# Performance work log

Measured on AMD Instinct MI355X. Metric: run time of the kernel, lower is better.

Reference implementation:

```python
import jax, jax.numpy as jnp
import numpy as np

N_NODES = 150000   # node_num
N_CENTROIDS = 256  # in_feats (must equal out_feats per source view())
EMBED = 256        # out_feats
EPS = 1e-7


def setup_inputs() -> dict:
    key = jax.random.key(0)
    k1, k2, k3 = jax.random.split(key, 3)
    x = jax.random.normal(k1, (N_NODES, EMBED), dtype=jnp.float32)
    # project node representations strictly inside the unit Poincare ball
    x = x / (1.0 + jnp.linalg.norm(x, axis=-1, keepdims=True)) * 0.9
    mask = (jax.random.uniform(k2, (N_NODES, 1)) < 0.9).astype(jnp.float32)
    # centroid_embedding init: uniform(-0.01, 0.01), already well inside the ball
    w = jax.random.uniform(k3, (N_CENTROIDS, EMBED), minval=-0.01, maxval=0.01,
                           dtype=jnp.float32)
    return {"node_repr": x, "mask": mask, "centroid_weight": w}


def _poincare_pairwise(x, c):
    # x: [N, D] inside unit ball, c: [C, D] inside unit ball -> [N, C]
    sx = jnp.sum(x * x, axis=-1)              # [N]
    sc = jnp.sum(c * c, axis=-1)              # [C]
    xc = x @ c.T                               # [N, C] (the only GEMM)
    sq = jnp.maximum(sx[:, None] + sc[None, :] - 2.0 * xc, 0.0)  # ||x-y||^2
    denom = jnp.maximum((1.0 - sx)[:, None] * (1.0 - sc)[None, :], 1e-12)
    arg = 1.0 + 2.0 * sq / denom
    return jnp.arccosh(jnp.maximum(arg, 1.0 + EPS))


def reference(node_repr, mask, centroid_weight):
    # node_repr: [N, D], mask: [N, 1], centroid_weight: [C, D]
    d = _poincare_pairwise(node_repr, centroid_weight)     # [N, C]
    node_centroid_dist = d[None, :, :] * mask              # [1, N, C] (mask broadcasts)
    graph_centroid_dist = jnp.sum(node_centroid_dist, axis=1) / jnp.sum(mask)  # [1, C]
    return graph_centroid_dist, node_centroid_dist
```

## Files before the change

kernel.cpp:

```cpp
#include <hip/hip_runtime.h>
#include <hip/hip_bf16.h>

#define N_NODES 150000
#define CDIM 256
#define DIM 256

typedef float f32x4 __attribute__((ext_vector_type(4)));
typedef short bf16x8 __attribute__((ext_vector_type(8)));

#define WS_CB 0
#define WS_SC 131072
#define WS_GACC 132096
#define WS_MSUM 133120

__device__ __forceinline__ unsigned short f2bf(float f) {
  unsigned u = __float_as_uint(f);
  u += 0x7FFFu + ((u >> 16) & 1u);
  return (unsigned short)(u >> 16);
}

__global__ void cd_prep(const float* __restrict__ cw, const float* __restrict__ mask,
                        unsigned short* __restrict__ cb, float* __restrict__ sc,
                        float* __restrict__ msum) {
  int b = blockIdx.x;
  int t = threadIdx.x;
  int wave = t >> 6, lane = t & 63;
  __shared__ float red[4];
  if (b < CDIM) {
    float v = cw[b * DIM + t];
    cb[(size_t)(t >> 3) * (CDIM * 8) + b * 8 + (t & 7)] = f2bf(v);
    float ss = v * v;
    #pragma unroll
    for (int off = 32; off >= 1; off >>= 1) ss += __shfl_xor(ss, off);
    if (lane == 0) red[wave] = ss;
    __syncthreads();
    if (t == 0) sc[b] = red[0] + red[1] + red[2] + red[3];
  } else {
    int idx = (b - CDIM) * 256 + t;
    const int stride = 64 * 256;
    float s = 0.f;
    for (int i = idx; i < N_NODES; i += stride) s += mask[i];
    #pragma unroll
    for (int off = 32; off >= 1; off >>= 1) s += __shfl_xor(s, off);
    if (lane == 0) red[wave] = s;
    __syncthreads();
    if (t == 0) atomicAdd(msum, red[0] + red[1] + red[2] + red[3]);
  }
}

__global__ __launch_bounds__(256, 2)
void cd_main(const float* __restrict__ x, const float* __restrict__ mask,
             const unsigned short* __restrict__ cb, const float* __restrict__ sc,
             float* __restrict__ gacc, float* __restrict__ out1) {
  const int lane = threadIdx.x & 63;
  const int w = threadIdx.x >> 6;
  const int q = lane >> 4;
  const int ln = lane & 15;
  const long m0 = (long)blockIdx.x * 64;
  const int c0 = w * 64;

  f32x4 acc[4][4] = {};
  float spart[4] = {0.f, 0.f, 0.f, 0.f};

  for (int kt = 0; kt < 8; ++kt) {
    bf16x8 bf[4];
    #pragma unroll
    for (int nt = 0; nt < 4; ++nt) {
      int col = c0 + nt * 16 + ln;
      bf[nt] = *(const bf16x8*)(cb + (size_t)(kt * 4 + q) * (CDIM * 8) + col * 8);
    }
    #pragma unroll
    for (int mt = 0; mt < 4; ++mt) {
      long row = m0 + mt * 16 + ln;
      long rg = row < N_NODES ? row : (long)(N_NODES - 1);
      const float* px = x + rg * DIM + kt * 32 + q * 8;
      f32x4 a0 = *(const f32x4*)px;
      f32x4 a1 = *(const f32x4*)(px + 4);
      spart[mt] += a0.x*a0.x + a0.y*a0.y + a0.z*a0.z + a0.w*a0.w
                 + a1.x*a1.x + a1.y*a1.y + a1.z*a1.z + a1.w*a1.w;
      bf16x8 af;
      af[0] = (short)f2bf(a0.x); af[1] = (short)f2bf(a0.y);
      af[2] = (short)f2bf(a0.z); af[3] = (short)f2bf(a0.w);
      af[4] = (short)f2bf(a1.x); af[5] = (short)f2bf(a1.y);
      af[6] = (short)f2bf(a1.z); af[7] = (short)f2bf(a1.w);
      #pragma unroll
      for (int nt = 0; nt < 4; ++nt)
        acc[mt][nt] = __builtin_amdgcn_mfma_f32_16x16x32_bf16(af, bf[nt], acc[mt][nt], 0, 0, 0);
    }
  }

  float sxv[4];
  #pragma unroll
  for (int mt = 0; mt < 4; ++mt) {
    float s = spart[mt];
    s += __shfl_xor(s, 16);
    s += __shfl_xor(s, 32);
    sxv[mt] = s;
  }

  float scv[4], rcv[4];
  #pragma unroll
  for (int nt = 0; nt < 4; ++nt) {
    scv[nt] = sc[c0 + nt * 16 + ln];
    rcv[nt] = 1.0f - scv[nt];
  }

  float pc[4] = {0.f, 0.f, 0.f, 0.f};
  #pragma unroll
  for (int mt = 0; mt < 4; ++mt) {
    float sxe[4], rxe[4], mke[4];
    long rows[4];
    #pragma unroll
    for (int i = 0; i < 4; ++i) {
      int rloc = q * 4 + i;
      sxe[i] = __shfl(sxv[mt], rloc);
      rows[i] = m0 + mt * 16 + rloc;
      mke[i] = (rows[i] < N_NODES) ? mask[rows[i]] : 0.f;
      rxe[i] = 1.0f - sxe[i];
    }
    #pragma unroll
    for (int nt = 0; nt < 4; ++nt) {
      int col = c0 + nt * 16 + ln;
      #pragma unroll
      for (int i = 0; i < 4; ++i) {
        float xc = acc[mt][nt][i];
        float sq = fmaf(-2.0f, xc, sxe[i] + scv[nt]);
        sq = fmaxf(sq, 0.0f);
        float den = fmaxf(rxe[i] * rcv[nt], 1e-12f);
        float z = 1.0f + __fdividef(2.0f * sq, den);
        z = fmaxf(z, 1.0f + 1e-7f);
        float t2 = z + sqrtf(fmaf(z, z, -1.0f));
        float dd = __log2f(t2) * 0.6931471805599453f;
        float o = dd * mke[i];
        if (rows[i] < N_NODES) out1[rows[i] * CDIM + col] = o;
        pc[nt] += o;
      }
    }
  }

  #pragma unroll
  for (int nt = 0; nt < 4; ++nt) {
    float s = pc[nt];
    s += __shfl_xor(s, 16);
    s += __shfl_xor(s, 32);
    if (lane < 16) atomicAdd(gacc + c0 + nt * 16 + ln, s);
  }
}

__global__ void cd_final(const float* __restrict__ gacc, const float* __restrict__ msum,
                         float* __restrict__ out0) {
  int t = threadIdx.x;
  out0[t] = gacc[t] / msum[0];
}

extern "C" void kernel_launch(void* const* d_in, const int* in_sizes, int n_in,
                              void* d_out, int out_size, void* d_ws, size_t ws_size,
                              hipStream_t stream) {
  const float* x    = (const float*)d_in[0];
  const float* mask = (const float*)d_in[1];
  const float* cw   = (const float*)d_in[2];
  float* out = (float*)d_out;
  char* ws = (char*)d_ws;
  unsigned short* cb = (unsigned short*)(ws + WS_CB);
  float* sc   = (float*)(ws + WS_SC);
  float* gacc = (float*)(ws + WS_GACC);
  float* msum = (float*)(ws + WS_MSUM);

  hipMemsetAsync(ws + WS_GACC, 0, 256 * 4 + 4, stream);
  cd_prep<<<320, 256, 0, stream>>>(cw, mask, cb, sc, msum);
  const int nblocks = (N_NODES + 63) / 64;
  cd_main<<<nblocks, 256, 0, stream>>>(x, mask, cb, sc, gacc, out + 256);
  cd_final<<<1, 256, 0, stream>>>(gacc, msum, out);
}
```

Baseline: 368.2 us.

## Stage bf16-converted node tile in LDS once per block, share across waves

```diff
diff --git a/kernel.cpp b/kernel.cpp
--- a/kernel.cpp
+++ b/kernel.cpp
@@ -7,6 +7,7 @@
 
 typedef float f32x4 __attribute__((ext_vector_type(4)));
 typedef short bf16x8 __attribute__((ext_vector_type(8)));
+typedef unsigned short u16x4 __attribute__((ext_vector_type(4)));
 
 #define WS_CB 0
 #define WS_SC 131072
@@ -48,54 +49,61 @@
   }
 }
 
-__global__ __launch_bounds__(256, 2)
+__global__ __launch_bounds__(256, 4)
 void cd_main(const float* __restrict__ x, const float* __restrict__ mask,
              const unsigned short* __restrict__ cb, const float* __restrict__ sc,
              float* __restrict__ gacc, float* __restrict__ out1) {
-  const int lane = threadIdx.x & 63;
-  const int w = threadIdx.x >> 6;
+  __shared__ unsigned short ab[32 * 64 * 8];
+  __shared__ float sxl[64];
+
+  const int t = threadIdx.x;
+  const long m0 = (long)blockIdx.x * 64;
+
+  {
+    const int row = t >> 2;
+    const int qq  = t & 3;
+    const long grow = m0 + row;
+    const bool ok = grow < N_NODES;
+    const float* px = x + grow * DIM;
+    float ss = 0.f;
+    #pragma unroll
+    for (int i = 0; i < 16; ++i) {
+      const int col4 = qq * 4 + i * 16;
+      f32x4 v;
+      if (ok) v = *(const f32x4*)(px + col4);
+      else    v = f32x4{0.f, 0.f, 0.f, 0.f};
+      ss = fmaf(v.x, v.x, ss); ss = fmaf(v.y, v.y, ss);
+      ss = fmaf(v.z, v.z, ss); ss = fmaf(v.w, v.w, ss);
+      u16x4 b;
+      b[0] = f2bf(v.x); b[1] = f2bf(v.y); b[2] = f2bf(v.z); b[3] = f2bf(v.w);
+      *(u16x4*)(ab + ((size_t)(col4 >> 3) * 64 + row) * 8 + (col4 & 7)) = b;
+    }
+    ss += __shfl_xor(ss, 1);
+    ss += __shfl_xor(ss, 2);
+    if (qq == 0) sxl[row] = ss;
+  }
+  __syncthreads();
+
+  const int lane = t & 63;
+  const int w = t >> 6;
   const int q = lane >> 4;
   const int ln = lane & 15;
-  const long m0 = (long)blockIdx.x * 64;
   const int c0 = w * 64;
 
   f32x4 acc[4][4] = {};
-  float spart[4] = {0.f, 0.f, 0.f, 0.f};
-
+  #pragma unroll
   for (int kt = 0; kt < 8; ++kt) {
     bf16x8 bf[4];
     #pragma unroll
-    for (int nt = 0; nt < 4; ++nt) {
-      int col = c0 + nt * 16 + ln;
-      bf[nt] = *(const bf16x8*)(cb + (size_t)(kt * 4 + q) * (CDIM * 8) + col * 8);
-    }
+    for (int nt = 0; nt < 4; ++nt)
+      bf[nt] = *(const bf16x8*)(cb + (size_t)(kt * 4 + q) * (CDIM * 8) + (c0 + nt * 16 + ln) * 8);
     #pragma unroll
     for (int mt = 0; mt < 4; ++mt) {
-      long row = m0 + mt * 16 + ln;
-      long rg = row < N_NODES ? row : (long)(N_NODES - 1);
-      const float* px = x + rg * DIM + kt * 32 + q * 8;
-      f32x4 a0 = *(const f32x4*)px;
-      f32x4 a1 = *(const f32x4*)(px + 4);
-      spart[mt] += a0.x*a0.x + a0.y*a0.y + a0.z*a0.z + a0.w*a0.w
-                 + a1.x*a1.x + a1.y*a1.y + a1.z*a1.z + a1.w*a1.w;
-      bf16x8 af;
-      af[0] = (short)f2bf(a0.x); af[1] = (short)f2bf(a0.y);
-      af[2] = (short)f2bf(a0.z); af[3] = (short)f2bf(a0.w);
-      af[4] = (short)f2bf(a1.x); af[5] = (short)f2bf(a1.y);
-      af[6] = (short)f2bf(a1.z); af[7] = (short)f2bf(a1.w);
+      bf16x8 af = *(const bf16x8*)(ab + ((size_t)(kt * 4 + q) * 64 + mt * 16 + ln) * 8);
       #pragma unroll
       for (int nt = 0; nt < 4; ++nt)
         acc[mt][nt] = __builtin_amdgcn_mfma_f32_16x16x32_bf16(af, bf[nt], acc[mt][nt], 0, 0, 0);
     }
-  }
-
-  float sxv[4];
-  #pragma unroll
-  for (int mt = 0; mt < 4; ++mt) {
-    float s = spart[mt];
-    s += __shfl_xor(s, 16);
-    s += __shfl_xor(s, 32);
-    sxv[mt] = s;
   }
 
   float scv[4], rcv[4];
@@ -112,15 +120,15 @@
     long rows[4];
     #pragma unroll
     for (int i = 0; i < 4; ++i) {
-      int rloc = q * 4 + i;
-      sxe[i] = __shfl(sxv[mt], rloc);
+      const int rloc = q * 4 + i;
+      sxe[i] = sxl[mt * 16 + rloc];
       rows[i] = m0 + mt * 16 + rloc;
       mke[i] = (rows[i] < N_NODES) ? mask[rows[i]] : 0.f;
       rxe[i] = 1.0f - sxe[i];
     }
     #pragma unroll
     for (int nt = 0; nt < 4; ++nt) {
-      int col = c0 + nt * 16 + ln;
+      const int col = c0 + nt * 16 + ln;
       #pragma unroll
       for (int i = 0; i < 4; ++i) {
         float xc = acc[mt][nt][i];
```

New measurement: 327.9 us. 11.0% less time.
